# Kernel optimization log

Hardware: AMD Instinct MI355X
Metric: run time of the kernel (lower is better)

The kernel has to match this reference:

```python
import jax, jax.numpy as jnp
import numpy as np

D_MODEL = 1024
N_HEADS = 16
POINT_DIM = 4
PLUCKER_DIM = 6
PAIRS4 = [(0, 1), (0, 2), (0, 3), (1, 2), (1, 3), (2, 3)]
_J6 = jnp.array([[0, 0, 0, 0, 0, 1], [0, 0, 0, 0, -1, 0], [0, 0, 0, 1, 0, 0],
                 [0, 0, 1, 0, 0, 0], [0, -1, 0, 0, 0, 0], [1, 0, 0, 0, 0, 0]], dtype=jnp.float32)


def exterior(p1, p2):
    # p1, p2: [..., point_dim] -> normalized Plucker coords [..., 6]
    L = jnp.stack([p1[..., i] * p2[..., j] - p1[..., j] * p2[..., i] for i, j in PAIRS4], axis=-1)
    n = jnp.linalg.norm(L, axis=-1, keepdims=True)
    return L / jnp.maximum(n, 1e-12)


def setup_inputs() -> dict:
    key = jax.random.key(0)
    ks = jax.random.split(key, 16)
    B, T, D, H, pd = 2, 1024, D_MODEL, N_HEADS, POINT_DIM
    s = 0.02
    return {
        "x": jax.random.normal(ks[0], (B, T, D), dtype=jnp.float32),
        "qkv_w": jax.random.normal(ks[1], (D, 3 * D), dtype=jnp.float32) * s,
        "qkv_b": jnp.zeros((3 * D,), dtype=jnp.float32),
        "w1_write_w": jax.random.normal(ks[2], (2 * D, pd * H), dtype=jnp.float32) * s,
        "w2_write_w": jax.random.normal(ks[3], (D, pd * H), dtype=jnp.float32) * s,
        "w1_read_w": jax.random.normal(ks[4], (D, pd * H), dtype=jnp.float32) * s,
        "w2_read_w": jax.random.normal(ks[5], (D, pd * H), dtype=jnp.float32) * s,
        "mem_value_w": jax.random.normal(ks[6], (D, D), dtype=jnp.float32) * s,
        "mem_value_b": jnp.zeros((D,), dtype=jnp.float32),
        "mem_gate_w": jax.random.normal(ks[7], (D, H), dtype=jnp.float32) * s,
        "mem_gate_b": jnp.zeros((H,), dtype=jnp.float32),
        "mem_scale": jnp.full((H,), 0.1, dtype=jnp.float32),
        "out_w": jax.random.normal(ks[8], (D, D), dtype=jnp.float32) * s,
        "out_b": jnp.zeros((D,), dtype=jnp.float32),
        "decay_logits": jnp.full((H,), 4.6, dtype=jnp.float32),
        "J": _J6,
    }


def reference(x, qkv_w, qkv_b, w1_write_w, w2_write_w, w1_read_w, w2_read_w,
              mem_value_w, mem_value_b, mem_gate_w, mem_gate_b, mem_scale,
              out_w, out_b, decay_logits, J):
    B, T, D = x.shape
    H = N_HEADS
    dh = D // H
    pd = POINT_DIM
    scale = dh ** (-0.5)

    # ---- standard causal attention ----
    qkv = (x @ qkv_w + qkv_b).reshape(B, T, 3, H, dh)
    q = jnp.transpose(qkv[:, :, 0], (0, 2, 1, 3))  # [B,H,T,dh]
    k = jnp.transpose(qkv[:, :, 1], (0, 2, 1, 3))
    v = jnp.transpose(qkv[:, :, 2], (0, 2, 1, 3))
    scores = jnp.einsum('bhtd,bhsd->bhts', q, k) * scale
    causal_mask = jnp.triu(jnp.ones((T, T), dtype=bool), k=1)
    scores = jnp.where(causal_mask, -jnp.inf, scores)
    attn = jax.nn.softmax(scores, axis=-1)
    seq_out = jnp.einsum('bhts,bhsd->bthd', attn, v).reshape(B, T, D)

    # ---- trigram write lines ----
    z = jnp.zeros((B, 1, D), dtype=x.dtype)
    x_prev1 = jnp.concatenate([z, x[:, :-1]], axis=1)
    x_prev2 = jnp.concatenate([z, z, x[:, :-2]], axis=1)
    trigram_ctx = jnp.concatenate([x_prev2, x_prev1], axis=-1)  # [B,T,2D]
    w1 = (trigram_ctx @ w1_write_w).reshape(B, T, H, pd)
    w2 = (x @ w2_write_w).reshape(B, T, H, pd)
    write_lines = exterior(w1, w2)  # [B,T,H,6]
    r1 = (x @ w1_read_w).reshape(B, T, H, pd)
    r2 = (x @ w2_read_w).reshape(B, T, H, pd)
    read_lines = exterior(r1, r2)  # [B,T,H,6]

    # ---- Plucker incidence + decay weighting ----
    J_write = jnp.einsum('bshi,ij->bshj', write_lines, J)
    incidence = jnp.einsum('bthi,bshi->bhts', read_lines, J_write)  # [B,H,T,T]
    incidence_sq = incidence ** 2
    positions = jnp.arange(T, dtype=x.dtype)
    diffs = positions[:, None] - positions[None, :]  # [T,T]
    decays = jax.nn.sigmoid(decay_logits)  # [H]
    # strictly-causal (diffs>0) decay weights; masked_fill(triu diag=0, 0) == (diffs>0)
    weights = jnp.where(diffs[None] > 0, decays[:, None, None] ** jnp.maximum(diffs, 0.0)[None], 0.0)
    mem_score = jnp.sum(incidence_sq * weights[None], axis=-1)  # [B,H,T]

    # ---- gated memory value ----
    mem_val = x @ mem_value_w + mem_value_b  # [B,T,D]
    gate = jax.nn.sigmoid(x @ mem_gate_w + mem_gate_b)  # [B,T,H]
    mem_score_t = jnp.transpose(mem_score, (0, 2, 1))  # [B,T,H]
    gated = jax.nn.sigmoid(mem_score_t * mem_scale[None, None, :]) * gate
    gated = jnp.mean(gated, axis=-1, keepdims=True)  # [B,T,1]

    return (seq_out + gated * mem_val) @ out_w + out_b
```

## Files before the change

### kernel.cpp

```cpp
#include <hip/hip_runtime.h>
#include <hip/hip_bf16.h>
#include <stdint.h>


typedef __attribute__((ext_vector_type(8))) __bf16 bf16v8;
typedef __attribute__((ext_vector_type(8))) short  s16x8;
typedef __attribute__((ext_vector_type(4))) float  f32x4;

#define LOG2E 1.4426950408889634f

__device__ __forceinline__ float bf2f(short s) {
  union { uint32_t u; float f; } cv; cv.u = ((uint32_t)(uint16_t)s) << 16; return cv.f;
}
__device__ __forceinline__ short f2bf(float f) {
  union { float f; uint32_t u; } cv; cv.f = f;
  uint32_t r = cv.u + 0x7fffu + ((cv.u >> 16) & 1u);
  return (short)(r >> 16);
}

__device__ __forceinline__ f32x4 mfma_bf16(s16x8 a, s16x8 b, f32x4 c) {
  return __builtin_amdgcn_mfma_f32_16x16x32_bf16(
      __builtin_bit_cast(bf16v8, a), __builtin_bit_cast(bf16v8, b), c, 0, 0, 0);
}

__device__ __forceinline__ void gload_lds16(const void* g, void* l) {
  __builtin_amdgcn_global_load_lds(
      (const __attribute__((address_space(1))) uint32_t*)g,
      (__attribute__((address_space(3))) uint32_t*)l, 16, 0, 0);
}


__global__ __launch_bounds__(256) void k_prep(
    const float* __restrict__ x, const float* __restrict__ qkvw,
    const float* __restrict__ mvw, const float* __restrict__ ow,
    const float* __restrict__ w1w, const float* __restrict__ w2w,
    const float* __restrict__ r1w, const float* __restrict__ r2w,
    const float* __restrict__ gw, const float* __restrict__ qkvb,
    const float* __restrict__ mvb,
    short* __restrict__ xb, short* __restrict__ btall, short* __restrict__ owT,
    float* __restrict__ biasAll) {
  __shared__ float tile[32][33];
  const int bid = blockIdx.x;
  const int tid = threadIdx.x;
  if (bid < 2048) {
    const int i = (bid * 256 + tid) * 4;
    float4 v = *(const float4*)&x[i];
    short4 o;
    o.x = f2bf(v.x); o.y = f2bf(v.y); o.z = f2bf(v.z); o.w = f2bf(v.w);
    *(short4*)&xb[i] = o;
    return;
  }
  if (bid < 7168) {
    const float* W; short* Wt; int N, u;
    if (bid < 5120)      { W = qkvw; Wt = btall;                       N = 3072; u = bid - 2048; }
    else if (bid < 6144) { W = mvw;  Wt = btall + (size_t)3072 * 1024; N = 1024; u = bid - 5120; }
    else                 { W = ow;   Wt = owT;                         N = 1024; u = bid - 6144; }
    const int ntiles = N >> 5;
    const int n0 = (u % ntiles) * 32, k0 = (u / ntiles) * 32;
    const int tx = tid & 31, ty = tid >> 5;
#pragma unroll
    for (int i = 0; i < 4; i++)
      tile[ty + i * 8][tx] = W[(size_t)(k0 + ty + i * 8) * N + n0 + tx];
    __syncthreads();
#pragma unroll
    for (int i = 0; i < 4; i++)
      Wt[(size_t)(n0 + ty + i * 8) * 1024 + k0 + tx] = f2bf(tile[tx][ty + i * 8]);
    return;
  }
  if (bid < 8704) {
    const int idx = (bid - 7168) * 256 + tid;
    const int r = idx >> 10, k = idx & 1023;
    float v = 0.f;
    if (r < 64)       v = w1w[(size_t)k * 64 + r];
    else if (r < 128) v = w1w[(size_t)(1024 + k) * 64 + (r - 64)];
    else if (r < 192) v = w2w[(size_t)k * 64 + (r - 128)];
    else if (r < 256) v = r1w[(size_t)k * 64 + (r - 192)];
    else if (r < 320) v = r2w[(size_t)k * 64 + (r - 256)];
    else if (r < 336) v = gw[(size_t)k * 16 + (r - 320)];
    btall[(size_t)4096 * 1024 + idx] = f2bf(v);
    return;
  }
  {
    const int i = (bid - 8704) * 256 + tid;
    if (i < 4480) {
      float v = 0.f;
      if (i < 3072) v = qkvb[i];
      else if (i < 4096) v = mvb[i - 3072];
      biasAll[i] = v;
    }
  }
}


__global__ __launch_bounds__(256) void k_gemmF(const short* __restrict__ A,
                                               const short* __restrict__ Bt,
                                               short* __restrict__ C,
                                               const float* __restrict__ bias,
                                               float* __restrict__ projf,
                                               short* __restrict__ vtg) {
  const int N = 4480, K = 1024;
  __shared__ short As[128 * 32];
  __shared__ short Bs[128 * 32];
  const int m0 = blockIdx.x * 128, n0 = blockIdx.y * 128;
  const int tid = threadIdx.x;
  const int lane = tid & 63, w = tid >> 6;
  const int wr = (w >> 1) * 64, wc = (w & 1) * 64;
  const int l15 = lane & 15, lg = lane >> 4;
  f32x4 acc[4][4] = {};
  for (int k0 = 0; k0 < K; k0 += 32) {
#pragma unroll
    for (int p = 0; p < 2; p++) {
      const int e = p * 256 + tid;
      const int r = e >> 2, c8 = (e & 3) << 3;
      gload_lds16(A + (size_t)(m0 + r) * K + k0 + c8, As + e * 8);
      gload_lds16(Bt + (size_t)(n0 + r) * K + k0 + c8, Bs + e * 8);
    }
    __syncthreads();
    s16x8 af[4], bfv[4];
#pragma unroll
    for (int i = 0; i < 4; i++) {
      af[i]  = *(const s16x8*)&As[(wr + i * 16 + l15) * 32 + lg * 8];
      bfv[i] = *(const s16x8*)&Bs[(wc + i * 16 + l15) * 32 + lg * 8];
    }
#pragma unroll
    for (int mi = 0; mi < 4; mi++)
#pragma unroll
      for (int ni = 0; ni < 4; ni++)
        acc[mi][ni] = mfma_bf16(af[mi], bfv[ni], acc[mi][ni]);
    __syncthreads();
  }
  const bool isproj = (n0 >= 4096);
  const bool isv = (n0 >= 2048) && (n0 < 3072);
#pragma unroll
  for (int mi = 0; mi < 4; mi++)
#pragma unroll
    for (int ni = 0; ni < 4; ni++) {
      const int col = n0 + wc + ni * 16 + l15;
      const float bv = bias[col];
      if (isv) {
        const int row0 = m0 + wr + mi * 16 + lg * 4;
        const int t0 = row0 & 1023, bloc = row0 >> 10;
        const int cd = col - 2048;
        const int hh = cd >> 6, dd = cd & 63;
        short4 pk;
        pk.x = f2bf(acc[mi][ni][0] + bv);
        pk.y = f2bf(acc[mi][ni][1] + bv);
        pk.z = f2bf(acc[mi][ni][2] + bv);
        pk.w = f2bf(acc[mi][ni][3] + bv);
        *(short4*)&vtg[((size_t)((bloc << 4) + hh) * 64 + dd) * 1024 + t0] = pk;
      } else {
#pragma unroll
        for (int r = 0; r < 4; r++) {
          const int row = m0 + wr + mi * 16 + lg * 4 + r;
          const float v = acc[mi][ni][r] + bv;
          if (isproj) projf[(size_t)row * 384 + (col - 4096)] = v;
          else        C[(size_t)row * 4480 + col] = f2bf(v);
        }
      }
    }
}


template <int BM>
__global__ __launch_bounds__(256) void k_gemm(const short* __restrict__ A,
                                              const short* __restrict__ Bt,
                                              float* __restrict__ C,
                                              const float* __restrict__ bias,
                                              int N, int K) {
  constexpr int MI = BM / 32;
  __shared__ short As[BM * 32];
  __shared__ short Bs[128 * 32];
  const int m0 = blockIdx.x * BM, n0 = blockIdx.y * 128;
  const int tid = threadIdx.x;
  const int lane = tid & 63, w = tid >> 6;
  const int wr = (w >> 1) * (BM / 2), wc = (w & 1) * 64;
  const int l15 = lane & 15, lg = lane >> 4;
  f32x4 acc[MI][4] = {};
  for (int k0 = 0; k0 < K; k0 += 32) {
    if constexpr (BM == 128) {
#pragma unroll
      for (int p = 0; p < 2; p++) {
        const int e = p * 256 + tid;
        const int r = e >> 2, c8 = (e & 3) << 3;
        gload_lds16(A + (size_t)(m0 + r) * K + k0 + c8, As + e * 8);
      }
    } else {
      const int r = tid >> 2, c8 = (tid & 3) << 3;
      gload_lds16(A + (size_t)(m0 + r) * K + k0 + c8, As + tid * 8);
    }
#pragma unroll
    for (int p = 0; p < 2; p++) {
      const int e = p * 256 + tid;
      const int r = e >> 2, c8 = (e & 3) << 3;
      gload_lds16(Bt + (size_t)(n0 + r) * K + k0 + c8, Bs + e * 8);
    }
    __syncthreads();
    s16x8 af[MI], bfv[4];
#pragma unroll
    for (int i = 0; i < MI; i++)
      af[i] = *(const s16x8*)&As[(wr + i * 16 + l15) * 32 + lg * 8];
#pragma unroll
    for (int i = 0; i < 4; i++)
      bfv[i] = *(const s16x8*)&Bs[(wc + i * 16 + l15) * 32 + lg * 8];
#pragma unroll
    for (int mi = 0; mi < MI; mi++)
#pragma unroll
      for (int ni = 0; ni < 4; ni++)
        acc[mi][ni] = mfma_bf16(af[mi], bfv[ni], acc[mi][ni]);
    __syncthreads();
  }
#pragma unroll
  for (int mi = 0; mi < MI; mi++)
#pragma unroll
    for (int ni = 0; ni < 4; ni++) {
      const int col = n0 + wc + ni * 16 + l15;
      const float bv = bias ? bias[col] : 0.f;
#pragma unroll
      for (int r = 0; r < 4; r++) {
        const int row = m0 + wr + mi * 16 + lg * 4 + r;
        C[(size_t)row * N + col] = acc[mi][ni][r] + bv;
      }
    }
}


__global__ __launch_bounds__(256) void k_attn(const short* __restrict__ fused,
                                              const short* __restrict__ vtg,
                                              float* __restrict__ Of,
                                              float* __restrict__ Ml) {
  const int id = blockIdx.x;
  const int j = 15 - (id >> 6);
  const int rem = id & 63;
  const int sid = rem >> 5, bh = rem & 31;
  const int b = bh >> 4, h = bh & 15;
  const int tid = threadIdx.x, lane = tid & 63, w = tid >> 6;
  const int l15 = lane & 15, lg = lane >> 4;
  const int q0 = j * 64;
  const int nkv = j + 1;
  const int half = (nkv + 1) >> 1;
  const int lo = sid ? half : 0;
  const int hi = sid ? nkv : half;
  const int pidx = ((j * 32 + bh) << 1) | sid;

  __shared__ short Kl[64 * 72];
  __shared__ short Vt[64 * 72];
  __shared__ short Pl[4][16 * 72];
  const short* base = fused + (size_t)b * 1024 * 4480;
  const short* vbase = vtg + (size_t)bh * 64 * 1024;

  const int e0 = tid, e1 = tid + 256;
  const int r0e = e0 >> 3, c0e = (e0 & 7) << 3;
  const int r1e = e1 >> 3, c1e = (e1 & 7) << 3;

  s16x8 qf[2];
#pragma unroll
  for (int ks = 0; ks < 2; ks++)
    qf[ks] = *(const s16x8*)&base[(size_t)(q0 + w * 16 + l15) * 4480 +
                                  h * 64 + ks * 32 + lg * 8];

  f32x4 O[4] = {};
  float m_run[4], l_run[4];
#pragma unroll
  for (int r = 0; r < 4; r++) { m_run[r] = -1e30f; l_run[r] = 0.f; }

  if (lo < hi) {
    const int kv0 = lo * 64;
    s16x8 ka = *(const s16x8*)&base[(size_t)(kv0 + r0e) * 4480 + 1024 + h * 64 + c0e];
    s16x8 kb = *(const s16x8*)&base[(size_t)(kv0 + r1e) * 4480 + 1024 + h * 64 + c1e];
    s16x8 va = *(const s16x8*)&vbase[(size_t)r0e * 1024 + kv0 + c0e];
    s16x8 vb = *(const s16x8*)&vbase[(size_t)r1e * 1024 + kv0 + c1e];
    *(s16x8*)&Kl[r0e * 72 + c0e] = ka;
    *(s16x8*)&Kl[r1e * 72 + c1e] = kb;
    *(s16x8*)&Vt[r0e * 72 + c0e] = va;
    *(s16x8*)&Vt[r1e * 72 + c1e] = vb;
  }
  __syncthreads();

  for (int kt = lo; kt < hi; kt++) {
    const int kv0 = kt * 64;
    const bool pf = (kt + 1 < hi);
    s16x8 kn0, kn1, vn0, vn1;
    if (pf) {
      const int kvn = kv0 + 64;
      kn0 = *(const s16x8*)&base[(size_t)(kvn + r0e) * 4480 + 1024 + h * 64 + c0e];
      kn1 = *(const s16x8*)&base[(size_t)(kvn + r1e) * 4480 + 1024 + h * 64 + c1e];
      vn0 = *(const s16x8*)&vbase[(size_t)r0e * 1024 + kvn + c0e];
      vn1 = *(const s16x8*)&vbase[(size_t)r1e * 1024 + kvn + c1e];
    }

    f32x4 S[4] = {};
    __builtin_amdgcn_s_setprio(1);
#pragma unroll
    for (int sf = 0; sf < 4; sf++) {
      s16x8 kf0 = *(const s16x8*)&Kl[(sf * 16 + l15) * 72 + lg * 8];
      s16x8 kf1 = *(const s16x8*)&Kl[(sf * 16 + l15) * 72 + 32 + lg * 8];
      S[sf] = mfma_bf16(qf[0], kf0, S[sf]);
      S[sf] = mfma_bf16(qf[1], kf1, S[sf]);
    }
    __builtin_amdgcn_s_setprio(0);

    const bool diag = (kt == j);
    float sv[4][4];
#pragma unroll
    for (int sf = 0; sf < 4; sf++)
#pragma unroll
      for (int r = 0; r < 4; r++) {
        float vv = S[sf][r] * 0.125f;
        if (diag) {
          const int sg = kv0 + sf * 16 + l15;
          const int qg = q0 + w * 16 + lg * 4 + r;
          if (sg > qg) vv = -1e30f;
        }
        sv[sf][r] = vv;
      }
#pragma unroll
    for (int r = 0; r < 4; r++) {
      float pm = fmaxf(fmaxf(sv[0][r], sv[1][r]), fmaxf(sv[2][r], sv[3][r]));
      pm = fmaxf(pm, __shfl_xor(pm, 1, 64));
      pm = fmaxf(pm, __shfl_xor(pm, 2, 64));
      pm = fmaxf(pm, __shfl_xor(pm, 4, 64));
      pm = fmaxf(pm, __shfl_xor(pm, 8, 64));
      if (pm > m_run[r] + 8.f) {
        const float fac = exp2f((m_run[r] - pm) * LOG2E);
        m_run[r] = pm;
        l_run[r] *= fac;
#pragma unroll
        for (int nf = 0; nf < 4; nf++) O[nf][r] *= fac;
      }
      float rs = 0.f;
#pragma unroll
      for (int sf = 0; sf < 4; sf++) {
        float p = (sv[sf][r] <= -1e29f) ? 0.f : exp2f((sv[sf][r] - m_run[r]) * LOG2E);
        rs += p;
        Pl[w][(lg * 4 + r) * 72 + sf * 16 + l15] = f2bf(p);
      }
      rs += __shfl_xor(rs, 1, 64);
      rs += __shfl_xor(rs, 2, 64);
      rs += __shfl_xor(rs, 4, 64);
      rs += __shfl_xor(rs, 8, 64);
      l_run[r] += rs;
    }

    __builtin_amdgcn_s_setprio(1);
#pragma unroll
    for (int ks = 0; ks < 2; ks++) {
      s16x8 pfr = *(const s16x8*)&Pl[w][l15 * 72 + ks * 32 + lg * 8];
#pragma unroll
      for (int nf = 0; nf < 4; nf++) {
        s16x8 vf = *(const s16x8*)&Vt[(nf * 16 + l15) * 72 + ks * 32 + lg * 8];
        O[nf] = mfma_bf16(pfr, vf, O[nf]);
      }
    }
    __builtin_amdgcn_s_setprio(0);

    __syncthreads();
    if (pf) {
      *(s16x8*)&Kl[r0e * 72 + c0e] = kn0;
      *(s16x8*)&Kl[r1e * 72 + c1e] = kn1;
      *(s16x8*)&Vt[r0e * 72 + c0e] = vn0;
      *(s16x8*)&Vt[r1e * 72 + c1e] = vn1;
      __syncthreads();
    }
  }

  float* ob = Of + (size_t)pidx * 4096;
  float* mb = Ml + (size_t)pidx * 128;
#pragma unroll
  for (int r = 0; r < 4; r++) {
    const int rloc = w * 16 + lg * 4 + r;
#pragma unroll
    for (int nf = 0; nf < 4; nf++)
      ob[rloc * 64 + nf * 16 + l15] = O[nf][r];
    if (l15 == 0) {
      mb[rloc] = m_run[r];
      mb[64 + rloc] = l_run[r];
    }
  }
}


__device__ __forceinline__ void exterior6(const float p1[4], const float p2[4], float L[6]) {
  L[0] = p1[0] * p2[1] - p1[1] * p2[0];
  L[1] = p1[0] * p2[2] - p1[2] * p2[0];
  L[2] = p1[0] * p2[3] - p1[3] * p2[0];
  L[3] = p1[1] * p2[2] - p1[2] * p2[1];
  L[4] = p1[1] * p2[3] - p1[3] * p2[1];
  L[5] = p1[2] * p2[3] - p1[3] * p2[2];
  float n = sqrtf(L[0] * L[0] + L[1] * L[1] + L[2] * L[2] +
                  L[3] * L[3] + L[4] * L[4] + L[5] * L[5]);
  float inv = 1.f / fmaxf(n, 1e-12f);
#pragma unroll
  for (int j = 0; j < 6; j++) L[j] *= inv;
}

__global__ void k_lines(const float* __restrict__ proj, const float* __restrict__ Jm,
                        float* __restrict__ jw, float* __restrict__ rl) {
  const int idx = blockIdx.x * 256 + threadIdx.x;
  const int t = idx & 1023, h = (idx >> 10) & 15, b = idx >> 14;
  const int n = b * 1024 + t;
  const int bh = b * 16 + h;
  float p1[4], p2[4], L[6];
#pragma unroll
  for (int p = 0; p < 4; p++) {
    float a  = (t >= 2) ? proj[(size_t)(n - 2) * 384 + h * 4 + p] : 0.f;
    float bb = (t >= 1) ? proj[(size_t)(n - 1) * 384 + 64 + h * 4 + p] : 0.f;
    p1[p] = a + bb;
    p2[p] = proj[(size_t)n * 384 + 128 + h * 4 + p];
  }
  exterior6(p1, p2, L);
  const size_t jo = (size_t)bh * 6144 + t;
#pragma unroll
  for (int j = 0; j < 6; j++) {
    float s = 0.f;
#pragma unroll
    for (int i = 0; i < 6; i++) s += L[i] * Jm[i * 6 + j];
    jw[jo + (size_t)j * 1024] = s;
  }
#pragma unroll
  for (int p = 0; p < 4; p++) {
    p1[p] = proj[(size_t)n * 384 + 192 + h * 4 + p];
    p2[p] = proj[(size_t)n * 384 + 256 + h * 4 + p];
  }
  exterior6(p1, p2, L);
  const size_t ro = ((size_t)bh * 1024 + t) * 6;
#pragma unroll
  for (int j = 0; j < 6; j++) rl[ro + j] = L[j];
}


__global__ __launch_bounds__(256) void k_mscore(const float* __restrict__ jw,
                                                const float* __restrict__ rl,
                                                const float* __restrict__ dlog,
                                                float* __restrict__ ms) {
  const int gtid = blockIdx.x * 256 + threadIdx.x;
  const int wid = gtid >> 6, lane = gtid & 63;
  const int bh = wid >> 10, t = wid & 1023;
  const int h = bh & 15, b = bh >> 4;
  const float d = 1.f / (1.f + expf(-dlog[h]));
  const float l2d = log2f(d);
  const float* jwp = jw + (size_t)bh * 6144;
  const float* rp = rl + ((size_t)bh * 1024 + t) * 6;
  const float r0 = rp[0], r1 = rp[1], r2 = rp[2], r3 = rp[3], r4 = rp[4], r5 = rp[5];
  float wgt = exp2f((float)(t - lane) * l2d);
  const float gw = exp2f(-64.f * l2d);
  float acc = 0.f;
  for (int s = lane; s < t; s += 64) {
    const float dot = r0 * jwp[s] + r1 * jwp[1024 + s] + r2 * jwp[2048 + s] +
                      r3 * jwp[3072 + s] + r4 * jwp[4096 + s] + r5 * jwp[5120 + s];
    acc += wgt * dot * dot;
    wgt *= gw;
  }
  acc += __shfl_xor(acc, 1, 64);
  acc += __shfl_xor(acc, 2, 64);
  acc += __shfl_xor(acc, 4, 64);
  acc += __shfl_xor(acc, 8, 64);
  acc += __shfl_xor(acc, 16, 64);
  acc += __shfl_xor(acc, 32, 64);
  if (lane == 0) ms[((size_t)(b * 1024 + t)) * 16 + h] = acc;
}


__global__ __launch_bounds__(256) void k_combine(const float* __restrict__ Of,
                                                 const float* __restrict__ Ml,
                                                 const short* __restrict__ fused,
                                                 const float* __restrict__ proj,
                                                 const float* __restrict__ ms,
                                                 const float* __restrict__ mem_scale,
                                                 const float* __restrict__ gate_b,
                                                 short* __restrict__ comb) {
  const int n = blockIdx.x;
  const int tid = threadIdx.x;
  __shared__ float gsh;
  if (tid < 16) {
    const float gp = proj[(size_t)n * 384 + 320 + tid] + gate_b[tid];
    const float g = 1.f / (1.f + expf(-gp));
    const float sc = ms[(size_t)n * 16 + tid] * mem_scale[tid];
    const float sg = 1.f / (1.f + expf(-sc));
    float v = sg * g;
    v += __shfl_xor(v, 1, 64);
    v += __shfl_xor(v, 2, 64);
    v += __shfl_xor(v, 4, 64);
    v += __shfl_xor(v, 8, 64);
    if (tid == 0) gsh = v * (1.f / 16.f);
  }
  __syncthreads();
  const float g = gsh;
  const int b = n >> 10, t = n & 1023;
  const int c0 = tid * 4;
  const int h = c0 >> 6, coff = c0 & 63;
  const int bh = b * 16 + h;
  const int p = ((t >> 6) * 32 + bh) << 1;
  const int rloc = t & 63;
  const float m0v = Ml[(size_t)p * 128 + rloc];
  const float l0v = Ml[(size_t)p * 128 + 64 + rloc];
  const float m1v = Ml[(size_t)(p + 1) * 128 + rloc];
  const float l1v = Ml[(size_t)(p + 1) * 128 + 64 + rloc];
  const float M = fmaxf(m0v, m1v);
  const float w0 = exp2f((m0v - M) * LOG2E);
  const float w1 = exp2f((m1v - M) * LOG2E);
  const float inv = 1.f / (w0 * l0v + w1 * l1v);
  f32x4 o0 = *(const f32x4*)&Of[(size_t)p * 4096 + rloc * 64 + coff];
  f32x4 o1 = *(const f32x4*)&Of[(size_t)(p + 1) * 4096 + rloc * 64 + coff];
  short4 mvv = *(const short4*)&fused[(size_t)n * 4480 + 3072 + c0];
  short4 ov;
  ov.x = f2bf((w0 * o0[0] + w1 * o1[0]) * inv + g * bf2f(mvv.x));
  ov.y = f2bf((w0 * o0[1] + w1 * o1[1]) * inv + g * bf2f(mvv.y));
  ov.z = f2bf((w0 * o0[2] + w1 * o1[2]) * inv + g * bf2f(mvv.z));
  ov.w = f2bf((w0 * o0[3] + w1 * o1[3]) * inv + g * bf2f(mvv.w));
  *(short4*)&comb[(size_t)n * 1024 + c0] = ov;
}


extern "C" void kernel_launch(void* const* d_in, const int* in_sizes, int n_in,
                              void* d_out, int out_size, void* d_ws, size_t ws_size,
                              hipStream_t stream) {
  const float* x    = (const float*)d_in[0];
  const float* qkvw = (const float*)d_in[1];
  const float* qkvb = (const float*)d_in[2];
  const float* w1w  = (const float*)d_in[3];
  const float* w2w  = (const float*)d_in[4];
  const float* r1w  = (const float*)d_in[5];
  const float* r2w  = (const float*)d_in[6];
  const float* mvw  = (const float*)d_in[7];
  const float* mvb  = (const float*)d_in[8];
  const float* gw   = (const float*)d_in[9];
  const float* gb   = (const float*)d_in[10];
  const float* msc  = (const float*)d_in[11];
  const float* ow   = (const float*)d_in[12];
  const float* ob   = (const float*)d_in[13];
  const float* dlog = (const float*)d_in[14];
  const float* Jm   = (const float*)d_in[15];
  float* out = (float*)d_out;

  char* wsp = (char*)d_ws;
  auto alloc = [&](size_t bytes) {
    char* p = wsp;
    wsp += (bytes + 255) & ~(size_t)255;
    return p;
  };
  short* xb     = (short*)alloc((size_t)2048 * 1024 * 2);
  short* btall  = (short*)alloc((size_t)4480 * 1024 * 2);
  short* owT    = (short*)alloc((size_t)1024 * 1024 * 2);
  short* fusedC = (short*)alloc((size_t)2048 * 4480 * 2);
  float* projf  = (float*)alloc((size_t)2048 * 384 * 4);
  float* biasA  = (float*)alloc((size_t)4480 * 4);
  short* vtg    = (short*)alloc((size_t)32 * 64 * 1024 * 2);
  short* comb   = (short*)alloc((size_t)2048 * 1024 * 2);
  float* jwb    = (float*)alloc((size_t)32 * 6144 * 4);
  float* rlb    = (float*)alloc((size_t)32768 * 6 * 4);
  float* msb    = (float*)alloc((size_t)2048 * 16 * 4);
  float* Of     = (float*)alloc((size_t)1024 * 4096 * 4);
  float* Mlb    = (float*)alloc((size_t)1024 * 128 * 4);

  k_prep<<<8722, 256, 0, stream>>>(x, qkvw, mvw, ow, w1w, w2w, r1w, r2w, gw,
                                   qkvb, mvb, xb, btall, owT, biasA);

  k_gemmF<<<dim3(16, 35), 256, 0, stream>>>(xb, btall, fusedC, biasA, projf, vtg);

  k_attn<<<1024, 256, 0, stream>>>(fusedC, vtg, Of, Mlb);

  k_lines<<<128, 256, 0, stream>>>(projf, Jm, jwb, rlb);
  k_mscore<<<8192, 256, 0, stream>>>(jwb, rlb, dlog, msb);
  k_combine<<<2048, 256, 0, stream>>>(Of, Mlb, fusedC, projf, msb, msc, gb, comb);

  k_gemm<64><<<dim3(32, 8), 256, 0, stream>>>(comb, owT, out, ob, 1024, 1024);
}
```

Baseline: 139.6 us.

## Double-buffer GEMM LDS tiles and move V transpose into a separate kernel

Both GEMM kernels now double-buffer their LDS tiles, so the next K-slice is prefetched while MFMAs run on the current one, and MFMA issue priority is raised with s_setprio. The V-transposed scatter store in the fused GEMM epilogue is removed and replaced by a dedicated LDS-tiled transpose kernel that reads V back from the fused output. This is meant to hide global-load latency and simplify the GEMM epilogue. In exchange it doubles LDS use per block, which may lower occupancy, and adds a kernel launch plus an extra read and write of V.

```diff
diff --git a/kernel.cpp b/kernel.cpp
--- a/kernel.cpp
+++ b/kernel.cpp
@@ -96,66 +96,64 @@
                                                const short* __restrict__ Bt,
                                                short* __restrict__ C,
                                                const float* __restrict__ bias,
-                                               float* __restrict__ projf,
-                                               short* __restrict__ vtg) {
+                                               float* __restrict__ projf) {
   const int N = 4480, K = 1024;
-  __shared__ short As[128 * 32];
-  __shared__ short Bs[128 * 32];
+  __shared__ short As[2][128 * 32];
+  __shared__ short Bs[2][128 * 32];
   const int m0 = blockIdx.x * 128, n0 = blockIdx.y * 128;
   const int tid = threadIdx.x;
   const int lane = tid & 63, w = tid >> 6;
   const int wr = (w >> 1) * 64, wc = (w & 1) * 64;
   const int l15 = lane & 15, lg = lane >> 4;
+  const int r0e = tid >> 2, c0e = (tid & 3) << 3;
+  const int r1e = (tid + 256) >> 2, c1e = ((tid + 256) & 3) << 3;
   f32x4 acc[4][4] = {};
-  for (int k0 = 0; k0 < K; k0 += 32) {
-#pragma unroll
-    for (int p = 0; p < 2; p++) {
-      const int e = p * 256 + tid;
-      const int r = e >> 2, c8 = (e & 3) << 3;
-      gload_lds16(A + (size_t)(m0 + r) * K + k0 + c8, As + e * 8);
-      gload_lds16(Bt + (size_t)(n0 + r) * K + k0 + c8, Bs + e * 8);
-    }
-    __syncthreads();
+
+  gload_lds16(A + (size_t)(m0 + r0e) * K + c0e, &As[0][tid * 8]);
+  gload_lds16(A + (size_t)(m0 + r1e) * K + c1e, &As[0][(tid + 256) * 8]);
+  gload_lds16(Bt + (size_t)(n0 + r0e) * K + c0e, &Bs[0][tid * 8]);
+  gload_lds16(Bt + (size_t)(n0 + r1e) * K + c1e, &Bs[0][(tid + 256) * 8]);
+  __syncthreads();
+
+  const int nkt = K >> 5;
+  for (int kt = 0; kt < nkt; kt++) {
+    const int cur = kt & 1;
+    if (kt + 1 < nkt) {
+      const int k0n = (kt + 1) << 5;
+      const int nxt = cur ^ 1;
+      gload_lds16(A + (size_t)(m0 + r0e) * K + k0n + c0e, &As[nxt][tid * 8]);
+      gload_lds16(A + (size_t)(m0 + r1e) * K + k0n + c1e, &As[nxt][(tid + 256) * 8]);
+      gload_lds16(Bt + (size_t)(n0 + r0e) * K + k0n + c0e, &Bs[nxt][tid * 8]);
+      gload_lds16(Bt + (size_t)(n0 + r1e) * K + k0n + c1e, &Bs[nxt][(tid + 256) * 8]);
+    }
     s16x8 af[4], bfv[4];
 #pragma unroll
     for (int i = 0; i < 4; i++) {
-      af[i]  = *(const s16x8*)&As[(wr + i * 16 + l15) * 32 + lg * 8];
-      bfv[i] = *(const s16x8*)&Bs[(wc + i * 16 + l15) * 32 + lg * 8];
-    }
+      af[i]  = *(const s16x8*)&As[cur][(wr + i * 16 + l15) * 32 + lg * 8];
+      bfv[i] = *(const s16x8*)&Bs[cur][(wc + i * 16 + l15) * 32 + lg * 8];
+    }
+    __builtin_amdgcn_s_setprio(1);
 #pragma unroll
     for (int mi = 0; mi < 4; mi++)
 #pragma unroll
       for (int ni = 0; ni < 4; ni++)
         acc[mi][ni] = mfma_bf16(af[mi], bfv[ni], acc[mi][ni]);
+    __builtin_amdgcn_s_setprio(0);
     __syncthreads();
   }
   const bool isproj = (n0 >= 4096);
-  const bool isv = (n0 >= 2048) && (n0 < 3072);
 #pragma unroll
   for (int mi = 0; mi < 4; mi++)
 #pragma unroll
     for (int ni = 0; ni < 4; ni++) {
       const int col = n0 + wc + ni * 16 + l15;
       const float bv = bias[col];
-      if (isv) {
-        const int row0 = m0 + wr + mi * 16 + lg * 4;
-        const int t0 = row0 & 1023, bloc = row0 >> 10;
-        const int cd = col - 2048;
-        const int hh = cd >> 6, dd = cd & 63;
-        short4 pk;
-        pk.x = f2bf(acc[mi][ni][0] + bv);
-        pk.y = f2bf(acc[mi][ni][1] + bv);
-        pk.z = f2bf(acc[mi][ni][2] + bv);
-        pk.w = f2bf(acc[mi][ni][3] + bv);
-        *(short4*)&vtg[((size_t)((bloc << 4) + hh) * 64 + dd) * 1024 + t0] = pk;
-      } else {
-#pragma unroll
-        for (int r = 0; r < 4; r++) {
-          const int row = m0 + wr + mi * 16 + lg * 4 + r;
-          const float v = acc[mi][ni][r] + bv;
-          if (isproj) projf[(size_t)row * 384 + (col - 4096)] = v;
-          else        C[(size_t)row * 4480 + col] = f2bf(v);
-        }
+#pragma unroll
+      for (int r = 0; r < 4; r++) {
+        const int row = m0 + wr + mi * 16 + lg * 4 + r;
+        const float v = acc[mi][ni][r] + bv;
+        if (isproj) projf[(size_t)row * 384 + (col - 4096)] = v;
+        else        C[(size_t)row * 4480 + col] = f2bf(v);
       }
     }
 }
@@ -168,45 +166,48 @@
                                               const float* __restrict__ bias,
                                               int N, int K) {
   constexpr int MI = BM / 32;
-  __shared__ short As[BM * 32];
-  __shared__ short Bs[128 * 32];
+  __shared__ short As[2][BM * 32];
+  __shared__ short Bs[2][128 * 32];
   const int m0 = blockIdx.x * BM, n0 = blockIdx.y * 128;
   const int tid = threadIdx.x;
   const int lane = tid & 63, w = tid >> 6;
   const int wr = (w >> 1) * (BM / 2), wc = (w & 1) * 64;
   const int l15 = lane & 15, lg = lane >> 4;
+  const int r0e = tid >> 2, c0e = (tid & 3) << 3;
+  const int r1e = (tid + 256) >> 2, c1e = ((tid + 256) & 3) << 3;
   f32x4 acc[MI][4] = {};
-  for (int k0 = 0; k0 < K; k0 += 32) {
+
+  auto stage = [&](int buf, int k0) {
     if constexpr (BM == 128) {
-#pragma unroll
-      for (int p = 0; p < 2; p++) {
-        const int e = p * 256 + tid;
-        const int r = e >> 2, c8 = (e & 3) << 3;
-        gload_lds16(A + (size_t)(m0 + r) * K + k0 + c8, As + e * 8);
-      }
+      gload_lds16(A + (size_t)(m0 + r0e) * K + k0 + c0e, &As[buf][tid * 8]);
+      gload_lds16(A + (size_t)(m0 + r1e) * K + k0 + c1e, &As[buf][(tid + 256) * 8]);
     } else {
-      const int r = tid >> 2, c8 = (tid & 3) << 3;
-      gload_lds16(A + (size_t)(m0 + r) * K + k0 + c8, As + tid * 8);
-    }
-#pragma unroll
-    for (int p = 0; p < 2; p++) {
-      const int e = p * 256 + tid;
-      const int r = e >> 2, c8 = (e & 3) << 3;
-      gload_lds16(Bt + (size_t)(n0 + r) * K + k0 + c8, Bs + e * 8);
-    }
-    __syncthreads();
+      gload_lds16(A + (size_t)(m0 + r0e) * K + k0 + c0e, &As[buf][tid * 8]);
+    }
+    gload_lds16(Bt + (size_t)(n0 + r0e) * K + k0 + c0e, &Bs[buf][tid * 8]);
+    gload_lds16(Bt + (size_t)(n0 + r1e) * K + k0 + c1e, &Bs[buf][(tid + 256) * 8]);
+  };
+
+  stage(0, 0);
+  __syncthreads();
+  const int nkt = K >> 5;
+  for (int kt = 0; kt < nkt; kt++) {
+    const int cur = kt & 1;
+    if (kt + 1 < nkt) stage(cur ^ 1, (kt + 1) << 5);
     s16x8 af[MI], bfv[4];
 #pragma unroll
     for (int i = 0; i < MI; i++)
-      af[i] = *(const s16x8*)&As[(wr + i * 16 + l15) * 32 + lg * 8];
+      af[i] = *(const s16x8*)&As[cur][(wr + i * 16 + l15) * 32 + lg * 8];
 #pragma unroll
     for (int i = 0; i < 4; i++)
-      bfv[i] = *(const s16x8*)&Bs[(wc + i * 16 + l15) * 32 + lg * 8];
+      bfv[i] = *(const s16x8*)&Bs[cur][(wc + i * 16 + l15) * 32 + lg * 8];
+    __builtin_amdgcn_s_setprio(1);
 #pragma unroll
     for (int mi = 0; mi < MI; mi++)
 #pragma unroll
       for (int ni = 0; ni < 4; ni++)
         acc[mi][ni] = mfma_bf16(af[mi], bfv[ni], acc[mi][ni]);
+    __builtin_amdgcn_s_setprio(0);
     __syncthreads();
   }
 #pragma unroll
@@ -221,6 +222,23 @@
         C[(size_t)row * N + col] = acc[mi][ni][r] + bv;
       }
     }
+}
+
+
+__global__ void k_vtr(const short* __restrict__ fused, short* __restrict__ vtg) {
+  __shared__ short tile[32][33];
+  const int bh = blockIdx.z;
+  const int b = bh >> 4, h = bh & 15;
+  const int t0 = blockIdx.x * 32, d0 = blockIdx.y * 32;
+  const int tx = threadIdx.x, ty = threadIdx.y;
+#pragma unroll
+  for (int i = 0; i < 4; i++)
+    tile[ty + i * 8][tx] =
+        fused[(size_t)(b * 1024 + t0 + ty + i * 8) * 4480 + 2048 + h * 64 + d0 + tx];
+  __syncthreads();
+#pragma unroll
+  for (int i = 0; i < 4; i++)
+    vtg[(size_t)(bh * 64 + d0 + ty + i * 8) * 1024 + t0 + tx] = tile[tx][ty + i * 8];
 }
 
 
@@ -555,8 +573,9 @@
   k_prep<<<8722, 256, 0, stream>>>(x, qkvw, mvw, ow, w1w, w2w, r1w, r2w, gw,
                                    qkvb, mvb, xb, btall, owT, biasA);
 
-  k_gemmF<<<dim3(16, 35), 256, 0, stream>>>(xb, btall, fusedC, biasA, projf, vtg);
-
+  k_gemmF<<<dim3(16, 35), 256, 0, stream>>>(xb, btall, fusedC, biasA, projf);
+
+  k_vtr<<<dim3(32, 2, 32), dim3(32, 8), 0, stream>>>(fusedC, vtg);
   k_attn<<<1024, 256, 0, stream>>>(fusedC, vtg, Of, Mlb);
 
   k_lines<<<128, 256, 0, stream>>>(projf, Jm, jwb, rlb);
```

New measurement: 126.9 us. 1.1x faster.
